# Optimization experiments

Measured on AMD Instinct MI355X. Metric: run time of the kernel, lower is better.

The kernel has to match this reference:

```python
import jax, jax.numpy as jnp
import numpy as np

N_NODES = 50000
IN_CH, HIDDEN, LATENT = 128, 256, 64
N_EDGES = 800000


def gcn_conv(x, edge_index, W, b, n_nodes):
    """PyG-style GCNConv: add self-loops, symmetric deg^{-1/2} normalization,
    linear transform, gather-scatter aggregation, bias."""
    loops = jnp.arange(n_nodes, dtype=edge_index.dtype)
    src = jnp.concatenate([edge_index[0], loops])  # [E+N]
    dst = jnp.concatenate([edge_index[1], loops])  # [E+N]
    deg = jax.ops.segment_sum(jnp.ones_like(dst, dtype=x.dtype), dst,
                              num_segments=n_nodes)  # [N]
    dinv = jnp.where(deg > 0, jax.lax.rsqrt(deg), 0.0)  # deg^{-1/2}
    h = x @ W  # [N, out] transform before propagation
    norm = dinv[src] * dinv[dst]  # [E+N]
    msg = h[src] * norm[:, None]  # gather + normalize, [E+N, out]
    out = jax.ops.segment_sum(msg, dst, num_segments=n_nodes)  # scatter-add
    return out + b


def setup_inputs() -> dict:
    key = jax.random.key(0)
    ks = jax.random.split(key, 10)
    x = jax.random.normal(ks[0], (N_NODES, IN_CH), dtype=jnp.float32)
    edge_index = jax.random.randint(ks[1], (2, N_EDGES), 0, N_NODES, dtype=jnp.int64)
    s = 0.05
    return {
        "x": x,
        "edge_index": edge_index,
        "W1": jax.random.normal(ks[2], (IN_CH, HIDDEN), dtype=jnp.float32) * s,
        "b1": jnp.zeros((HIDDEN,), dtype=jnp.float32),
        "W2": jax.random.normal(ks[3], (HIDDEN, LATENT), dtype=jnp.float32) * s,
        "b2": jnp.zeros((LATENT,), dtype=jnp.float32),
        "Wd1": jax.random.normal(ks[4], (LATENT, HIDDEN), dtype=jnp.float32) * s,
        "bd1": jnp.zeros((HIDDEN,), dtype=jnp.float32),
        "Wd2": jax.random.normal(ks[5], (HIDDEN, IN_CH), dtype=jnp.float32) * s,
        "bd2": jnp.zeros((IN_CH,), dtype=jnp.float32),
    }


def reference(x, edge_index, W1, b1, W2, b2, Wd1, bd1, Wd2, bd2):
    n = x.shape[0]
    # Encoder: two GCN layers
    h = jax.nn.relu(gcn_conv(x, edge_index, W1, b1, n))
    z = gcn_conv(h, edge_index, W2, b2, n)
    # Decoder: dense MLP
    d = jax.nn.relu(z @ Wd1 + bd1)
    return d @ Wd2 + bd2
```

## Files before the change

kernel.cpp:

```cpp
#include <hip/hip_runtime.h>


#define IN_CH  128
#define HIDDEN 256
#define LATENT 64
#define CAP    64

typedef unsigned short u16;
typedef unsigned int u32;
typedef float f32x4 __attribute__((ext_vector_type(4)));
typedef _Float16 f16x4 __attribute__((ext_vector_type(4)));
typedef _Float16 f16x8 __attribute__((ext_vector_type(8)));

static __device__ __forceinline__ float4 ld4(const float* p) {
    return *reinterpret_cast<const float4*>(p);
}
static __device__ __forceinline__ void acc4(float4& a, float4 v) {
    a.x += v.x; a.y += v.y; a.z += v.z; a.w += v.w;
}
static __device__ __forceinline__ f16x4 ldh4(const _Float16* p) {
    return *reinterpret_cast<const f16x4*>(p);
}
static __device__ __forceinline__ void acch(float4& a, f16x4 v) {
    a.x += (float)v[0]; a.y += (float)v[1]; a.z += (float)v[2]; a.w += (float)v[3];
}

static __device__ __forceinline__ long tix(int row, int k, int K) {
    return ((long)(row >> 4) * (K >> 3) + (k >> 3)) * 128 + ((row & 15) << 3) + (k & 7);
}

#define MFMA16(ACC, A, B)                                                      \
    ACC = __builtin_amdgcn_mfma_f32_16x16x32_f16(A, B, ACC, 0, 0, 0);


__global__ void fill_kernel(const int* __restrict__ ei, int E,
                            int* __restrict__ cnt, int* __restrict__ col, int nper) {
    int part = blockIdx.x & 7;
    int e = (blockIdx.x >> 3) * 256 + threadIdx.x;
    if (e >= E) return;
    int d = ei[E + e];
    if ((unsigned)(d - part * nper) < (unsigned)nper) {
        int pos = atomicAdd(&cnt[d], 1);
        col[d * CAP + pos] = ei[e];
    }
}

__global__ void prep_kernel(
    const int* __restrict__ cnt, const float* __restrict__ x,
    float* __restrict__ dinv, _Float16* __restrict__ xsh, int N, int total4, int pblk,
    const float* __restrict__ W1, const float* __restrict__ W2,
    const float* __restrict__ Wd1, const float* __restrict__ Wd2,
    _Float16* __restrict__ w1f, _Float16* __restrict__ w2f,
    _Float16* __restrict__ wd1f, _Float16* __restrict__ wd2f) {
    if ((int)blockIdx.x < pblk) {
        int i = blockIdx.x * 256 + threadIdx.x;
        if (i < total4) {
            int node = i >> 5;
            float dv = rsqrtf((float)cnt[node] + 1.0f);
            if ((i & 31) == 0) dinv[node] = dv;
            float4 v = ld4(&x[(long)i * 4]);
            f16x4 h;
            h[0] = (_Float16)(v.x * dv);
            h[1] = (_Float16)(v.y * dv);
            h[2] = (_Float16)(v.z * dv);
            h[3] = (_Float16)(v.w * dv);
            *reinterpret_cast<f16x4*>(&xsh[(long)i * 4]) = h;
        }
    } else {
        int idx = ((int)blockIdx.x - pblk) * 256 + threadIdx.x;
        if (idx < 98304) {
            const float* W; _Float16* H; int K, Nn, base;
            if (idx < 32768)      { W = W1;  H = w1f;  K = 128; Nn = 256; base = idx; }
            else if (idx < 49152) { W = W2;  H = w2f;  K = 256; Nn = 64;  base = idx - 32768; }
            else if (idx < 65536) { W = Wd1; H = wd1f; K = 64;  Nn = 256; base = idx - 49152; }
            else                  { W = Wd2; H = wd2f; K = 256; Nn = 128; base = idx - 65536; }
            int k = base / Nn, n = base % Nn;
            H[tix(n, k, K)] = (_Float16)W[base];
        }
    }
}


__global__ __launch_bounds__(256) void aggx_kernel(
    const _Float16* __restrict__ xsh, const int* __restrict__ cnt,
    const int* __restrict__ col, const float* __restrict__ dinv,
    _Float16* __restrict__ xaf, int N) {
    int wid = threadIdx.x >> 6;
    int lane = threadIdx.x & 63;
    int node = blockIdx.x * 4 + wid;
    if (node >= N) return;
    int slot = lane >> 5;
    int c = (lane & 31) * 4;

    float4 a0 = make_float4(0.f, 0.f, 0.f, 0.f);
    float4 a1 = a0, a2 = a0, a3 = a0;
    if (slot == 0) acch(a0, ldh4(&xsh[(long)node * 128 + c]));

    int deg = cnt[node];
    int cb = node * CAP;
    {
        int cv = (lane < deg) ? col[cb + lane] : 0;
        int full = deg >> 1;
        int trips = (deg + 1) >> 1;
        int t = 0;
        for (; t + 4 <= full; t += 4) {
            int j = slot + 2 * t;
            int s0 = __shfl(cv, j);
            int s1 = __shfl(cv, j + 2);
            int s2 = __shfl(cv, j + 4);
            int s3 = __shfl(cv, j + 6);
            f16x4 v0 = ldh4(&xsh[(long)s0 * 128 + c]);
            f16x4 v1 = ldh4(&xsh[(long)s1 * 128 + c]);
            f16x4 v2 = ldh4(&xsh[(long)s2 * 128 + c]);
            f16x4 v3 = ldh4(&xsh[(long)s3 * 128 + c]);
            acch(a0, v0); acch(a1, v1); acch(a2, v2); acch(a3, v3);
        }
        for (; t < trips; t++) {
            int j = slot + 2 * t;
            bool p = j < deg;
            int s = __shfl(cv, p ? j : 0);
            if (p) acch(a0, ldh4(&xsh[(long)s * 128 + c]));
        }
    }
    acc4(a0, a1); acc4(a2, a3); acc4(a0, a2);
    a0.x += __shfl_xor(a0.x, 32);
    a0.y += __shfl_xor(a0.y, 32);
    a0.z += __shfl_xor(a0.z, 32);
    a0.w += __shfl_xor(a0.w, 32);
    if (slot == 0) {
        float di = dinv[node];
        f16x4 h;
        h[0] = (_Float16)(a0.x * di);
        h[1] = (_Float16)(a0.y * di);
        h[2] = (_Float16)(a0.z * di);
        h[3] = (_Float16)(a0.w * di);
        *(f16x4*)&xaf[tix(node, c, 128)] = h;
    }
}

__global__ __launch_bounds__(256) void agg64_kernel(
    const _Float16* __restrict__ zsh, const int* __restrict__ cnt,
    const int* __restrict__ col, const float* __restrict__ dinv,
    const float* __restrict__ bias,
    _Float16* __restrict__ zf, int N) {
    int wid = threadIdx.x >> 6;
    int lane = threadIdx.x & 63;
    int node = blockIdx.x * 4 + wid;
    if (node >= N) return;
    int slot = lane >> 4;
    int c = (lane & 15) * 4;

    float4 a0 = make_float4(0.f, 0.f, 0.f, 0.f);
    float4 a1 = a0, a2 = a0, a3 = a0;
    if (slot == 0) acch(a0, ldh4(&zsh[(long)node * 64 + c]));

    int deg = cnt[node];
    int cb = node * CAP;
    {
        int cv = (lane < deg) ? col[cb + lane] : 0;
        int full = deg >> 2;
        int trips = (deg + 3) >> 2;
        int t = 0;
        for (; t + 4 <= full; t += 4) {
            int j = slot + 4 * t;
            int s0 = __shfl(cv, j);
            int s1 = __shfl(cv, j + 4);
            int s2 = __shfl(cv, j + 8);
            int s3 = __shfl(cv, j + 12);
            f16x4 v0 = ldh4(&zsh[(long)s0 * 64 + c]);
            f16x4 v1 = ldh4(&zsh[(long)s1 * 64 + c]);
            f16x4 v2 = ldh4(&zsh[(long)s2 * 64 + c]);
            f16x4 v3 = ldh4(&zsh[(long)s3 * 64 + c]);
            acch(a0, v0); acch(a1, v1); acch(a2, v2); acch(a3, v3);
        }
        for (; t < trips; t++) {
            int j = slot + 4 * t;
            bool p = j < deg;
            int s = __shfl(cv, p ? j : 0);
            if (p) acch(a0, ldh4(&zsh[(long)s * 64 + c]));
        }
    }
    acc4(a0, a1); acc4(a2, a3); acc4(a0, a2);
    a0.x += __shfl_xor(a0.x, 16); a0.x += __shfl_xor(a0.x, 32);
    a0.y += __shfl_xor(a0.y, 16); a0.y += __shfl_xor(a0.y, 32);
    a0.z += __shfl_xor(a0.z, 16); a0.z += __shfl_xor(a0.z, 32);
    a0.w += __shfl_xor(a0.w, 16); a0.w += __shfl_xor(a0.w, 32);
    if (slot == 0) {
        float di = dinv[node];
        float4 bi = ld4(&bias[c]);
        f16x4 h;
        h[0] = (_Float16)(a0.x * di + bi.x);
        h[1] = (_Float16)(a0.y * di + bi.y);
        h[2] = (_Float16)(a0.z * di + bi.z);
        h[3] = (_Float16)(a0.w * di + bi.w);
        *(f16x4*)&zf[tix(node, c, 64)] = h;
    }
}

__global__ __launch_bounds__(256) void enc_fused(
    const _Float16* __restrict__ xaf,
    const _Float16* __restrict__ w1f, const _Float16* __restrict__ w2f,
    const float* __restrict__ b1, const float* __restrict__ dinv,
    _Float16* __restrict__ zsh, int M) {
    __shared__ _Float16 o1f[32 * 256];

    const int tid = threadIdx.x;
    const int wid = tid >> 6, lane = tid & 63, quad = lane >> 4, lm = lane & 15;
    const int rt0 = blockIdx.x * 2;
    const int last_rt = (M >> 4) - 1;

    f32x4 acc[2][4];
#pragma unroll
    for (int i = 0; i < 2; i++)
#pragma unroll
        for (int j = 0; j < 4; j++) acc[i][j] = (f32x4){0.f, 0.f, 0.f, 0.f};

#pragma unroll
    for (int kc = 0; kc < 4; kc++) {
        const int kb = kc * 4 + quad;
        f16x8 a[2], b[4];
#pragma unroll
        for (int i = 0; i < 2; i++) {
            int rt = rt0 + i; rt = rt <= last_rt ? rt : last_rt;
            long o = ((long)rt * 16 + kb) * 128 + lm * 8;
            a[i] = *(const f16x8*)&xaf[o];
        }
#pragma unroll
        for (int j = 0; j < 4; j++) {
            long o = ((long)(wid * 4 + j) * 16 + kb) * 128 + lm * 8;
            b[j] = *(const f16x8*)&w1f[o];
        }
#pragma unroll
        for (int i = 0; i < 2; i++)
#pragma unroll
            for (int j = 0; j < 4; j++) { MFMA16(acc[i][j], a[i], b[j]); }
    }

#pragma unroll
    for (int i = 0; i < 2; i++)
#pragma unroll
        for (int j = 0; j < 4; j++) {
            int coln = wid * 64 + j * 16 + lm;
            float bi = b1[coln];
#pragma unroll
            for (int r = 0; r < 4; r++) {
                int row = i * 16 + quad * 4 + r;
                float v = fmaxf(acc[i][j][r] + bi, 0.f);
                int o = ((row >> 4) * 32 + (coln >> 3)) * 128 + ((row & 15) << 3) + (coln & 7);
                o1f[o] = (_Float16)v;
            }
        }
    __syncthreads();

    f32x4 acc2[2];
    acc2[0] = (f32x4){0.f, 0.f, 0.f, 0.f};
    acc2[1] = (f32x4){0.f, 0.f, 0.f, 0.f};
#pragma unroll
    for (int kc = 0; kc < 8; kc++) {
        const int kb = kc * 4 + quad;
        f16x8 a[2], b;
#pragma unroll
        for (int i = 0; i < 2; i++) {
            int o = (i * 32 + kb) * 128 + lm * 8;
            a[i] = *(const f16x8*)&o1f[o];
        }
        {
            long o = ((long)wid * 32 + kb) * 128 + lm * 8;
            b = *(const f16x8*)&w2f[o];
        }
#pragma unroll
        for (int i = 0; i < 2; i++) { MFMA16(acc2[i], a[i], b); }
    }
#pragma unroll
    for (int i = 0; i < 2; i++) {
        int coln = wid * 16 + lm;
#pragma unroll
        for (int r = 0; r < 4; r++) {
            int row = rt0 * 16 + i * 16 + quad * 4 + r;
            if (row < M) zsh[(long)row * 64 + coln] = (_Float16)(acc2[i][r] * dinv[row]);
        }
    }
}

__global__ __launch_bounds__(256) void dec_fused(
    const _Float16* __restrict__ zf,
    const _Float16* __restrict__ wd1f, const _Float16* __restrict__ wd2f,
    const float* __restrict__ bd1, const float* __restrict__ bd2,
    float* __restrict__ out, int M) {
    __shared__ _Float16 dsm[32 * 256];

    const int tid = threadIdx.x;
    const int wid = tid >> 6, lane = tid & 63, quad = lane >> 4, lm = lane & 15;
    const int rt0 = blockIdx.x * 2;
    const int last_rt = (M >> 4) - 1;

    f32x4 acc[2][4];
#pragma unroll
    for (int i = 0; i < 2; i++)
#pragma unroll
        for (int j = 0; j < 4; j++) acc[i][j] = (f32x4){0.f, 0.f, 0.f, 0.f};

#pragma unroll
    for (int kc = 0; kc < 2; kc++) {
        const int kb = kc * 4 + quad;
        f16x8 a[2], b[4];
#pragma unroll
        for (int i = 0; i < 2; i++) {
            int rt = rt0 + i; rt = rt <= last_rt ? rt : last_rt;
            long o = ((long)rt * 8 + kb) * 128 + lm * 8;
            a[i] = *(const f16x8*)&zf[o];
        }
#pragma unroll
        for (int j = 0; j < 4; j++) {
            long o = ((long)(wid * 4 + j) * 8 + kb) * 128 + lm * 8;
            b[j] = *(const f16x8*)&wd1f[o];
        }
#pragma unroll
        for (int i = 0; i < 2; i++)
#pragma unroll
            for (int j = 0; j < 4; j++) { MFMA16(acc[i][j], a[i], b[j]); }
    }

#pragma unroll
    for (int i = 0; i < 2; i++)
#pragma unroll
        for (int j = 0; j < 4; j++) {
            int coln = wid * 64 + j * 16 + lm;
            float bi = bd1[coln];
#pragma unroll
            for (int r = 0; r < 4; r++) {
                int row = i * 16 + quad * 4 + r;
                float v = fmaxf(acc[i][j][r] + bi, 0.f);
                int o = ((row >> 4) * 32 + (coln >> 3)) * 128 + ((row & 15) << 3) + (coln & 7);
                dsm[o] = (_Float16)v;
            }
        }
    __syncthreads();

    f32x4 acc2[2][2];
#pragma unroll
    for (int i = 0; i < 2; i++)
#pragma unroll
        for (int j = 0; j < 2; j++) acc2[i][j] = (f32x4){0.f, 0.f, 0.f, 0.f};
#pragma unroll
    for (int kc = 0; kc < 8; kc++) {
        const int kb = kc * 4 + quad;
        f16x8 a[2], b[2];
#pragma unroll
        for (int i = 0; i < 2; i++) {
            int o = (i * 32 + kb) * 128 + lm * 8;
            a[i] = *(const f16x8*)&dsm[o];
        }
#pragma unroll
        for (int j = 0; j < 2; j++) {
            long o = ((long)(wid * 2 + j) * 32 + kb) * 128 + lm * 8;
            b[j] = *(const f16x8*)&wd2f[o];
        }
#pragma unroll
        for (int i = 0; i < 2; i++)
#pragma unroll
            for (int j = 0; j < 2; j++) { MFMA16(acc2[i][j], a[i], b[j]); }
    }
#pragma unroll
    for (int i = 0; i < 2; i++)
#pragma unroll
        for (int j = 0; j < 2; j++) {
            int coln = wid * 32 + j * 16 + lm;
            float bi = bd2[coln];
#pragma unroll
            for (int r = 0; r < 4; r++) {
                int row = rt0 * 16 + i * 16 + quad * 4 + r;
                if (row < M) out[(long)row * 128 + coln] = acc2[i][j][r] + bi;
            }
        }
}


extern "C" void kernel_launch(void* const* d_in, const int* in_sizes, int n_in,
                              void* d_out, int out_size, void* d_ws, size_t ws_size,
                              hipStream_t stream) {
    const float* x        = (const float*)d_in[0];
    const int* ei         = (const int*)d_in[1];
    const float* W1       = (const float*)d_in[2];
    const float* b1       = (const float*)d_in[3];
    const float* W2       = (const float*)d_in[4];
    const float* b2       = (const float*)d_in[5];
    const float* Wd1      = (const float*)d_in[6];
    const float* bd1      = (const float*)d_in[7];
    const float* Wd2      = (const float*)d_in[8];
    const float* bd2      = (const float*)d_in[9];
    float* out            = (float*)d_out;

    const int N = in_sizes[0] / IN_CH;
    const int E = in_sizes[1] / 2;

    char* p = (char*)d_ws;
    auto alloc = [&](size_t bytes) {
        char* r = p;
        p += (bytes + 255) & ~(size_t)255;
        return r;
    };
    int*      cnt       = (int*)     alloc((size_t)N * 4);
    float*    dinv      = (float*)   alloc((size_t)N * 4);
    int*      col       = (int*)     alloc((size_t)N * CAP * 4);
    _Float16* xsh       = (_Float16*)alloc((size_t)N * IN_CH * 2);
    _Float16* xaf       = (_Float16*)alloc((size_t)N * IN_CH * 2);
    _Float16* zsh       = (_Float16*)alloc((size_t)N * LATENT * 2);
    _Float16* zf        = (_Float16*)alloc((size_t)N * LATENT * 2);
    _Float16* w1f       = (_Float16*)alloc((size_t)IN_CH * HIDDEN * 2);
    _Float16* w2f       = (_Float16*)alloc((size_t)HIDDEN * LATENT * 2);
    _Float16* wd1f      = (_Float16*)alloc((size_t)LATENT * HIDDEN * 2);
    _Float16* wd2f      = (_Float16*)alloc((size_t)HIDDEN * IN_CH * 2);

    const int total4 = N * (IN_CH / 4);
    const int chunks = (E + 255) / 256;
    const int nper = (N + 7) / 8;
    const int fblk = (N + 31) / 32;
    const int pblk = (total4 + 255) / 256;

    hipMemsetAsync(cnt, 0, (size_t)N * 4, stream);
    fill_kernel<<<chunks * 8, 256, 0, stream>>>(ei, E, cnt, col, nper);
    prep_kernel<<<pblk + 384, 256, 0, stream>>>(
        cnt, x, dinv, xsh, N, total4, pblk,
        W1, W2, Wd1, Wd2, w1f, w2f, wd1f, wd2f);

    aggx_kernel<<<(N + 3) / 4, 256, 0, stream>>>(xsh, cnt, col, dinv, xaf, N);
    enc_fused<<<fblk, 256, 0, stream>>>(xaf, w1f, w2f, b1, dinv, zsh, N);
    agg64_kernel<<<(N + 3) / 4, 256, 0, stream>>>(zsh, cnt, col, dinv, b2, zf, N);
    dec_fused<<<fblk, 256, 0, stream>>>(zf, wd1f, wd2f, bd1, bd2, out, N);
}
```

Baseline: 219.6 us.

## Split per-node adjacency buckets into sub-buckets to cut atomic contention in fill

Edge bucketing now writes into 8 sub-buckets per destination node (selected by block index), each holding 16 slots. Each edge is therefore read once, replacing the earlier 8 partitioned passes over the edge list, and atomics on a node's counter are spread across sub-counters. Aggregation kernels compact the sub-buckets into a per-wave shared-memory index list using ballot/popcount before gathering. The cost is larger counter and column arrays, an extra compaction step in both aggregation passes, and silent edge drops if a sub-bucket receives more than 16 entries, while the degree used for normalisation still counts every edge.

```diff
diff --git a/kernel.cpp b/kernel.cpp
--- a/kernel.cpp
+++ b/kernel.cpp
@@ -4,10 +4,12 @@
 #define IN_CH  128
 #define HIDDEN 256
 #define LATENT 64
-#define CAP    64
+#define SUBS   8
+#define SLOTS  16
 
 typedef unsigned short u16;
 typedef unsigned int u32;
+typedef unsigned long long u64;
 typedef float f32x4 __attribute__((ext_vector_type(4)));
 typedef _Float16 f16x4 __attribute__((ext_vector_type(4)));
 typedef _Float16 f16x8 __attribute__((ext_vector_type(8)));
@@ -34,15 +36,13 @@
 
 
 __global__ void fill_kernel(const int* __restrict__ ei, int E,
-                            int* __restrict__ cnt, int* __restrict__ col, int nper) {
-    int part = blockIdx.x & 7;
-    int e = (blockIdx.x >> 3) * 256 + threadIdx.x;
+                            int* __restrict__ cnt, int* __restrict__ col) {
+    int e = blockIdx.x * 256 + threadIdx.x;
     if (e >= E) return;
+    int sub = blockIdx.x & 7;
     int d = ei[E + e];
-    if ((unsigned)(d - part * nper) < (unsigned)nper) {
-        int pos = atomicAdd(&cnt[d], 1);
-        col[d * CAP + pos] = ei[e];
-    }
+    int pos = atomicAdd(&cnt[d * SUBS + sub], 1);
+    if (pos < SLOTS) col[d * (SUBS * SLOTS) + sub * SLOTS + pos] = ei[e];
 }
 
 __global__ void prep_kernel(
@@ -56,7 +56,10 @@
         int i = blockIdx.x * 256 + threadIdx.x;
         if (i < total4) {
             int node = i >> 5;
-            float dv = rsqrtf((float)cnt[node] + 1.0f);
+            const int4* c4 = reinterpret_cast<const int4*>(&cnt[node * SUBS]);
+            int4 ca = c4[0], cb = c4[1];
+            int deg = ca.x + ca.y + ca.z + ca.w + cb.x + cb.y + cb.z + cb.w;
+            float dv = rsqrtf((float)deg + 1.0f);
             if ((i & 31) == 0) dinv[node] = dv;
             float4 v = ld4(&x[(long)i * 4]);
             f16x4 h;
@@ -80,47 +83,65 @@
     }
 }
 
+static __device__ __forceinline__ int compact_bucket(
+    const int* __restrict__ cnt, const int* __restrict__ col,
+    int node, int lane, int* buf) {
+    int deg = 0;
+#pragma unroll
+    for (int i = 0; i < 2; i++) {
+        int idx = i * 64 + lane;
+        int sub = idx >> 4, slot = idx & 15;
+        int sc = cnt[node * SUBS + sub];
+        bool valid = slot < (sc < SLOTS ? sc : SLOTS);
+        int cv = col[node * (SUBS * SLOTS) + idx];
+        u64 m = __ballot(valid);
+        int base = __popcll(m & ((1ull << lane) - 1ull));
+        if (valid) buf[deg + base] = cv;
+        deg += (int)__popcll(m);
+    }
+    return deg;
+}
+
 
 __global__ __launch_bounds__(256) void aggx_kernel(
     const _Float16* __restrict__ xsh, const int* __restrict__ cnt,
     const int* __restrict__ col, const float* __restrict__ dinv,
     _Float16* __restrict__ xaf, int N) {
+    __shared__ int idxbuf[4][128];
     int wid = threadIdx.x >> 6;
     int lane = threadIdx.x & 63;
     int node = blockIdx.x * 4 + wid;
     if (node >= N) return;
     int slot = lane >> 5;
     int c = (lane & 31) * 4;
+    int* buf = idxbuf[wid];
+
+    int deg = compact_bucket(cnt, col, node, lane, buf);
 
     float4 a0 = make_float4(0.f, 0.f, 0.f, 0.f);
     float4 a1 = a0, a2 = a0, a3 = a0;
     if (slot == 0) acch(a0, ldh4(&xsh[(long)node * 128 + c]));
 
-    int deg = cnt[node];
-    int cb = node * CAP;
-    {
-        int cv = (lane < deg) ? col[cb + lane] : 0;
-        int full = deg >> 1;
-        int trips = (deg + 1) >> 1;
-        int t = 0;
-        for (; t + 4 <= full; t += 4) {
-            int j = slot + 2 * t;
-            int s0 = __shfl(cv, j);
-            int s1 = __shfl(cv, j + 2);
-            int s2 = __shfl(cv, j + 4);
-            int s3 = __shfl(cv, j + 6);
-            f16x4 v0 = ldh4(&xsh[(long)s0 * 128 + c]);
-            f16x4 v1 = ldh4(&xsh[(long)s1 * 128 + c]);
-            f16x4 v2 = ldh4(&xsh[(long)s2 * 128 + c]);
-            f16x4 v3 = ldh4(&xsh[(long)s3 * 128 + c]);
-            acch(a0, v0); acch(a1, v1); acch(a2, v2); acch(a3, v3);
-        }
-        for (; t < trips; t++) {
-            int j = slot + 2 * t;
-            bool p = j < deg;
-            int s = __shfl(cv, p ? j : 0);
-            if (p) acch(a0, ldh4(&xsh[(long)s * 128 + c]));
-        }
+    int full = deg >> 1;
+    int trips = (deg + 1) >> 1;
+    int t = 0;
+    for (; t + 4 <= full; t += 4) {
+        int j = slot + 2 * t;
+        int s0 = buf[j];
+        int s1 = buf[j + 2];
+        int s2 = buf[j + 4];
+        int s3 = buf[j + 6];
+        f16x4 v0 = ldh4(&xsh[(long)s0 * 128 + c]);
+        f16x4 v1 = ldh4(&xsh[(long)s1 * 128 + c]);
+        f16x4 v2 = ldh4(&xsh[(long)s2 * 128 + c]);
+        f16x4 v3 = ldh4(&xsh[(long)s3 * 128 + c]);
+        acch(a0, v0); acch(a1, v1); acch(a2, v2); acch(a3, v3);
+    }
+    for (; t < trips; t++) {
+        int j = slot + 2 * t;
+        bool p = j < deg;
+        int s = buf[p ? j : 0];
+        if (p) acch(a0, ldh4(&xsh[(long)s * 128 + c]));
     }
     acc4(a0, a1); acc4(a2, a3); acc4(a0, a2);
     a0.x += __shfl_xor(a0.x, 32);
@@ -143,42 +164,41 @@
     const int* __restrict__ col, const float* __restrict__ dinv,
     const float* __restrict__ bias,
     _Float16* __restrict__ zf, int N) {
+    __shared__ int idxbuf[4][128];
     int wid = threadIdx.x >> 6;
     int lane = threadIdx.x & 63;
     int node = blockIdx.x * 4 + wid;
     if (node >= N) return;
     int slot = lane >> 4;
     int c = (lane & 15) * 4;
+    int* buf = idxbuf[wid];
+
+    int deg = compact_bucket(cnt, col, node, lane, buf);
 
     float4 a0 = make_float4(0.f, 0.f, 0.f, 0.f);
     float4 a1 = a0, a2 = a0, a3 = a0;
     if (slot == 0) acch(a0, ldh4(&zsh[(long)node * 64 + c]));
 
-    int deg = cnt[node];
-    int cb = node * CAP;
-    {
-        int cv = (lane < deg) ? col[cb + lane] : 0;
-        int full = deg >> 2;
-        int trips = (deg + 3) >> 2;
-        int t = 0;
-        for (; t + 4 <= full; t += 4) {
-            int j = slot + 4 * t;
-            int s0 = __shfl(cv, j);
-            int s1 = __shfl(cv, j + 4);
-            int s2 = __shfl(cv, j + 8);
-            int s3 = __shfl(cv, j + 12);
-            f16x4 v0 = ldh4(&zsh[(long)s0 * 64 + c]);
-            f16x4 v1 = ldh4(&zsh[(long)s1 * 64 + c]);
-            f16x4 v2 = ldh4(&zsh[(long)s2 * 64 + c]);
-            f16x4 v3 = ldh4(&zsh[(long)s3 * 64 + c]);
-            acch(a0, v0); acch(a1, v1); acch(a2, v2); acch(a3, v3);
-        }
-        for (; t < trips; t++) {
-            int j = slot + 4 * t;
-            bool p = j < deg;
-            int s = __shfl(cv, p ? j : 0);
-            if (p) acch(a0, ldh4(&zsh[(long)s * 64 + c]));
-        }
+    int full = deg >> 2;
+    int trips = (deg + 3) >> 2;
+    int t = 0;
+    for (; t + 4 <= full; t += 4) {
+        int j = slot + 4 * t;
+        int s0 = buf[j];
+        int s1 = buf[j + 4];
+        int s2 = buf[j + 8];
+        int s3 = buf[j + 12];
+        f16x4 v0 = ldh4(&zsh[(long)s0 * 64 + c]);
+        f16x4 v1 = ldh4(&zsh[(long)s1 * 64 + c]);
+        f16x4 v2 = ldh4(&zsh[(long)s2 * 64 + c]);
+        f16x4 v3 = ldh4(&zsh[(long)s3 * 64 + c]);
+        acch(a0, v0); acch(a1, v1); acch(a2, v2); acch(a3, v3);
+    }
+    for (; t < trips; t++) {
+        int j = slot + 4 * t;
+        bool p = j < deg;
+        int s = buf[p ? j : 0];
+        if (p) acch(a0, ldh4(&zsh[(long)s * 64 + c]));
     }
     acc4(a0, a1); acc4(a2, a3); acc4(a0, a2);
     a0.x += __shfl_xor(a0.x, 16); a0.x += __shfl_xor(a0.x, 32);
@@ -400,9 +420,9 @@
         p += (bytes + 255) & ~(size_t)255;
         return r;
     };
-    int*      cnt       = (int*)     alloc((size_t)N * 4);
+    int*      cnt       = (int*)     alloc((size_t)N * SUBS * 4);
     float*    dinv      = (float*)   alloc((size_t)N * 4);
-    int*      col       = (int*)     alloc((size_t)N * CAP * 4);
+    int*      col       = (int*)     alloc((size_t)N * SUBS * SLOTS * 4);
     _Float16* xsh       = (_Float16*)alloc((size_t)N * IN_CH * 2);
     _Float16* xaf       = (_Float16*)alloc((size_t)N * IN_CH * 2);
     _Float16* zsh       = (_Float16*)alloc((size_t)N * LATENT * 2);
@@ -414,12 +434,11 @@
 
     const int total4 = N * (IN_CH / 4);
     const int chunks = (E + 255) / 256;
-    const int nper = (N + 7) / 8;
     const int fblk = (N + 31) / 32;
     const int pblk = (total4 + 255) / 256;
 
-    hipMemsetAsync(cnt, 0, (size_t)N * 4, stream);
-    fill_kernel<<<chunks * 8, 256, 0, stream>>>(ei, E, cnt, col, nper);
+    hipMemsetAsync(cnt, 0, (size_t)N * SUBS * 4, stream);
+    fill_kernel<<<chunks, 256, 0, stream>>>(ei, E, cnt, col);
     prep_kernel<<<pblk + 384, 256, 0, stream>>>(
         cnt, x, dinv, xsh, N, total4, pblk,
         W1, W2, Wd1, Wd2, w1f, w2f, wd1f, wd2f);
```

Measured after the change: 237.5 us. 8.1% more time.
